# Kernel tuning notes

Measured on AMD Instinct MI355X. Metric: run time of the kernel, lower is better.

## Reference

```python
import jax, jax.numpy as jnp
import numpy as np

# dims
B, L = 2, 1024            # batch, seq len (queries == keys)
DQ, DK, DSRC = 1024, 1024, 512
VIEWS, WIDTH, TOPK = 8, 4, 8
DVP = DQ // VIEWS         # per-view head dim = 128
PAD_F = (WIDTH - 1) // 2  # dilocal 'same' zero padding (stride=1, dilation=1)
PAD_B = (WIDTH - 1) - PAD_F


def setup_inputs() -> dict:
    key = jax.random.key(0)
    ks = jax.random.split(key, 5)
    s = 0.02
    return {
        "query": jax.random.normal(ks[0], (B, L, DQ), jnp.float32),
        "key_t": jax.random.normal(ks[1], (B, L, DK), jnp.float32),
        "source": jax.random.normal(ks[2], (B, L, DSRC), jnp.float32),
        "wq": jax.random.normal(ks[3], (VIEWS, DVP, DQ), jnp.float32) * s,
        "bq": jnp.zeros((VIEWS, DVP), jnp.float32),
        "wk": jax.random.normal(ks[4], (VIEWS, DVP, DK), jnp.float32) * s,
        "bk": jnp.zeros((VIEWS, DVP), jnp.float32),
    }


def reference(query, key_t, source, wq, bq, wk, bk):
    # --- ViewPointFactory.forward ---
    # multi-view projections: [B, L, D] -> [B, views, L, dvp]
    q = jnp.einsum('bld,vkd->bvlk', query, wq) + bq[None, :, None, :]
    k = jnp.einsum('bld,vkd->bvlk', key_t, wk) + bk[None, :, None, :]
    # attention scores over all keys: [B, views, Lq, Lk] (no sqrt(d) scaling in source)
    score = jnp.einsum('bvqd,bvkd->bvqk', q, k)
    # torch.sort(descending) + slice == top_k with sorted values
    vals, idx = jax.lax.top_k(score, TOPK)          # [B, views, Lq, TOPK]
    weights = jax.nn.softmax(vals, axis=-1)

    # --- ViewPoint.__call__(source) ---
    # dilocal: width-WIDTH local windows, stride 1, dilation 1, zero 'same' pad
    padded = jnp.pad(source, ((0, 0), (PAD_F, PAD_B), (0, 0)))
    win_idx = jnp.arange(L)[:, None] + jnp.arange(WIDTH)[None, :]  # [L, WIDTH]
    windows = padded[:, win_idx, :]                 # [B, L, WIDTH, DSRC]

    # gather the top-k key windows per (view, query): [B, views, Lq, TOPK, WIDTH, DSRC]
    gathered = jax.vmap(lambda w, i: w[i])(windows, idx)
    # weighted sum over top-k -> [B, views, Lq, WIDTH, DSRC]
    out = jnp.einsum('bvqk,bvqkwd->bvqwd', weights, gathered)
    return out
```

## Files before the change

kernel.cpp:

```cpp
#include <hip/hip_runtime.h>
#include <cstdint>

#define L_SEQ 1024
#define DSRC 512
#define XPL 2097152L
#define WPL 1048576L

typedef __attribute__((ext_vector_type(8))) short short8;
typedef __attribute__((ext_vector_type(4))) float floatx4;

__device__ __forceinline__ unsigned short f2bf(float f) {
  unsigned int x = __float_as_uint(f);
  x += 0x7fff + ((x >> 16) & 1);
  return (unsigned short)(x >> 16);
}
__device__ __forceinline__ float bf2f(unsigned short h) {
  return __uint_as_float((unsigned)h << 16);
}
__device__ __forceinline__ void split3(float f, unsigned short* h) {
  h[0] = f2bf(f);
  float d = f - bf2f(h[0]);
  h[1] = f2bf(d);
  h[2] = f2bf(d - bf2f(h[1]));
}

__device__ __forceinline__ void gload_lds16(const void* g, void* l) {
  __builtin_amdgcn_global_load_lds(
      (const __attribute__((address_space(1))) unsigned int*)g,
      (__attribute__((address_space(3))) unsigned int*)l, 16, 0, 0);
}

__global__ __launch_bounds__(256) void split_inputs_k(
    const float* __restrict__ query, const float* __restrict__ key_t,
    const float* __restrict__ wq, const float* __restrict__ wk,
    ushort* __restrict__ xs, ushort* __restrict__ wsp) {
  int blk = blockIdx.x;
  const float* in; ushort* out; long pl; int idx;
  if (blk < 2048)      { in = query; out = xs;           pl = XPL; idx = blk; }
  else if (blk < 4096) { in = key_t; out = xs + 3 * XPL; pl = XPL; idx = blk - 2048; }
  else if (blk < 5120) { in = wq;    out = wsp;          pl = WPL; idx = blk - 4096; }
  else                 { in = wk;    out = wsp + 3 * WPL; pl = WPL; idx = blk - 5120; }
  long e = (long)idx * 1024 + threadIdx.x * 4;
  float4 v = *(const float4*)(in + e);
  unsigned short h0[3], h1[3], h2[3], h3[3];
  split3(v.x, h0); split3(v.y, h1); split3(v.z, h2); split3(v.w, h3);
#pragma unroll
  for (int s = 0; s < 3; s++) {
    ushort4 u; u.x = h0[s]; u.y = h1[s]; u.z = h2[s]; u.w = h3[s];
    *(ushort4*)(out + s * pl + e) = u;
  }
}

__global__ __launch_bounds__(512, 2) void proj_gemm_k(
    const ushort* __restrict__ xs, const ushort* __restrict__ wsp,
    ushort* __restrict__ qs, ushort* __restrict__ ks,
    const float* __restrict__ bq, const float* __restrict__ bk) {
  __shared__ ushort As[2][3][4096];
  __shared__ ushort Bs[2][3][4096];
  int z = blockIdx.z;
  const ushort* Ab = xs + (long)z * 3 * XPL + (long)blockIdx.y * 128 * 1024;
  const ushort* Bb = wsp + (long)z * 3 * WPL + (long)blockIdx.x * 128 * 1024;

  int tid = threadIdx.x;
  int lane = tid & 63, wv = tid >> 6;
  int wm = wv >> 2, wn = wv & 3;
  int quad = lane >> 4, l16 = lane & 15;

  int sr = tid >> 2;
  int scq = (((tid & 3) ^ ((sr >> 1) & 3)) << 3);

  floatx4 acc[4][2] = {};

#pragma unroll
  for (int s = 0; s < 3; s++) {
    gload_lds16(Ab + (long)s * XPL + (long)sr * 1024 + scq, &As[0][s][wv * 512]);
    gload_lds16(Bb + (long)s * WPL + (long)sr * 1024 + scq, &Bs[0][s][wv * 512]);
  }
  __syncthreads();

  int cur = 0;
#pragma unroll 2
  for (int t = 0; t < 32; t++) {
    if (t < 31) {
      int k0 = (t + 1) * 32;
#pragma unroll
      for (int s = 0; s < 3; s++) {
        gload_lds16(Ab + (long)s * XPL + (long)sr * 1024 + k0 + scq, &As[cur ^ 1][s][wv * 512]);
        gload_lds16(Bb + (long)s * WPL + (long)sr * 1024 + k0 + scq, &Bs[cur ^ 1][s][wv * 512]);
      }
    }
    short8 af[3][4];
#pragma unroll
    for (int s = 0; s < 3; s++)
#pragma unroll
      for (int i = 0; i < 4; i++) {
        int row = wm * 64 + i * 16 + l16;
        int qa = (quad ^ ((row >> 1) & 3)) << 3;
        af[s][i] = *(const short8*)(&As[cur][s][row * 32 + qa]);
      }
#pragma unroll
    for (int j = 0; j < 2; j++) {
      int rowb = wn * 32 + j * 16 + l16;
      int boff = rowb * 32 + ((quad ^ ((rowb >> 1) & 3)) << 3);
      short8 b0 = *(const short8*)(&Bs[cur][0][boff]);
      short8 b1 = *(const short8*)(&Bs[cur][1][boff]);
      short8 b2 = *(const short8*)(&Bs[cur][2][boff]);
#pragma unroll
      for (int i = 0; i < 4; i++) {
        acc[i][j] = __builtin_amdgcn_mfma_f32_16x16x32_bf16(af[1][i], b1, acc[i][j], 0, 0, 0);
        acc[i][j] = __builtin_amdgcn_mfma_f32_16x16x32_bf16(af[0][i], b2, acc[i][j], 0, 0, 0);
        acc[i][j] = __builtin_amdgcn_mfma_f32_16x16x32_bf16(af[2][i], b0, acc[i][j], 0, 0, 0);
        acc[i][j] = __builtin_amdgcn_mfma_f32_16x16x32_bf16(af[0][i], b1, acc[i][j], 0, 0, 0);
        acc[i][j] = __builtin_amdgcn_mfma_f32_16x16x32_bf16(af[1][i], b0, acc[i][j], 0, 0, 0);
        acc[i][j] = __builtin_amdgcn_mfma_f32_16x16x32_bf16(af[0][i], b0, acc[i][j], 0, 0, 0);
      }
    }
    __syncthreads();
    cur ^= 1;
  }

  ushort* Ob = z ? ks : qs;
  const float* bias = z ? bk : bq;
#pragma unroll
  for (int j = 0; j < 2; j++) {
    int col = blockIdx.x * 128 + wn * 32 + j * 16 + l16;
    float bv = bias[col];
#pragma unroll
    for (int i = 0; i < 4; i++) {
#pragma unroll
      for (int r = 0; r < 4; r++) {
        long row = blockIdx.y * 128 + wm * 64 + i * 16 + quad * 4 + r;
        float val = acc[i][j][r] + bv;
        unsigned short h[3]; split3(val, h);
        long e = row * 1024 + col;
#pragma unroll
        for (int s = 0; s < 3; s++) Ob[s * XPL + e] = h[s];
      }
    }
  }
}

__global__ __launch_bounds__(512) void score_topk_k(
    const ushort* __restrict__ qs, const ushort* __restrict__ ks,
    float* __restrict__ wts, int* __restrict__ idxs) {
  __shared__ ushort Asm[3 * 64 * 128];
  __shared__ ushort Bsm[2][3 * 128 * 32];
  __shared__ float  Ssm[64 * 132];

  int fid = blockIdx.x + 16 * (blockIdx.y + 8 * blockIdx.z);
  int xcd = fid & 7, jj = fid >> 3;
  int pair = xcd * 2 + (jj & 1);
  int rt = jj >> 1;
  int v = pair & 7, b = pair >> 3;

  const long arow0 = (long)b * 1024 + rt * 64;
  const long brow0 = (long)b * 1024;
  const int vb = v * 128;

  int tid = threadIdx.x;
  int lane = tid & 63, wv = tid >> 6;
  int wm = wv >> 2, wn = wv & 3;
  int quad = lane >> 4, l16 = lane & 15;

#pragma unroll
  for (int n = 0; n < 6; n++) {
    int base = n * 512 + wv * 64;
    int sl = base + lane;
    int s = sl >> 10, rem = sl & 1023;
    int r = rem >> 4, sq = rem & 15;
    int qb = sq ^ (r & 7);
    gload_lds16(qs + (long)s * XPL + (arow0 + r) * 1024 + vb + qb * 8,
                &Asm[base * 8]);
  }

  auto stageB = [&](int step, int bsel) {
    int ct2 = step >> 2, kk2 = step & 3;
    long kb = brow0 + ct2 * 128;
    int k0 = kk2 * 32;
#pragma unroll
    for (int n = 0; n < 3; n++) {
      int base = n * 512 + wv * 64;
      int sl = base + lane;
      int s = sl >> 9, rem = sl & 511;
      int c = rem >> 2, sq = rem & 3;
      int qb = sq ^ ((c >> 1) & 3);
      gload_lds16(ks + (long)s * XPL + (kb + c) * 1024 + vb + k0 + qb * 8,
                  &Bsm[bsel][base * 8]);
    }
  };

  stageB(0, 0);
  __syncthreads();

  floatx4 acc[2][2] = {};
  float rv = -1e30f; int rc = 0x7FFFFFFF;
  const int myrow = tid >> 3, lc = tid & 7;

  int buf = 0;
  for (int ct = 0; ct < 8; ct++) {
#pragma unroll
    for (int kk = 0; kk < 4; kk++) {
      int step = ct * 4 + kk;
      if (step < 31) stageB(step + 1, buf ^ 1);

      short8 af[3][2], bf[3][2];
#pragma unroll
      for (int s = 0; s < 3; s++)
#pragma unroll
        for (int i = 0; i < 2; i++) {
          int row = wm * 32 + i * 16 + l16;
          int sqa = (kk * 4 + quad) ^ (row & 7);
          af[s][i] = *(const short8*)(&Asm[s * 8192 + row * 128 + sqa * 8]);
        }
#pragma unroll
      for (int s = 0; s < 3; s++)
#pragma unroll
        for (int j = 0; j < 2; j++) {
          int c = wn * 32 + j * 16 + l16;
          int sqb = quad ^ ((c >> 1) & 3);
          bf[s][j] = *(const short8*)(&Bsm[buf][s * 4096 + c * 32 + sqb * 8]);
        }
#pragma unroll
      for (int j = 0; j < 2; j++)
#pragma unroll
        for (int i = 0; i < 2; i++) {
          acc[i][j] = __builtin_amdgcn_mfma_f32_16x16x32_bf16(af[1][i], bf[1][j], acc[i][j], 0, 0, 0);
          acc[i][j] = __builtin_amdgcn_mfma_f32_16x16x32_bf16(af[0][i], bf[2][j], acc[i][j], 0, 0, 0);
          acc[i][j] = __builtin_amdgcn_mfma_f32_16x16x32_bf16(af[2][i], bf[0][j], acc[i][j], 0, 0, 0);
          acc[i][j] = __builtin_amdgcn_mfma_f32_16x16x32_bf16(af[0][i], bf[1][j], acc[i][j], 0, 0, 0);
          acc[i][j] = __builtin_amdgcn_mfma_f32_16x16x32_bf16(af[1][i], bf[0][j], acc[i][j], 0, 0, 0);
          acc[i][j] = __builtin_amdgcn_mfma_f32_16x16x32_bf16(af[0][i], bf[0][j], acc[i][j], 0, 0, 0);
        }
      __syncthreads();
      buf ^= 1;
    }

#pragma unroll
    for (int i = 0; i < 2; i++)
#pragma unroll
      for (int j = 0; j < 2; j++)
#pragma unroll
        for (int r = 0; r < 4; r++) {
          int row = wm * 32 + i * 16 + quad * 4 + r;
          int col = wn * 32 + j * 16 + l16;
          Ssm[row * 132 + col] = acc[i][j][r];
          acc[i][j][r] = 0.0f;
        }
    __syncthreads();

    float vv[16];
#pragma unroll
    for (int t = 0; t < 16; t++) vv[t] = Ssm[myrow * 132 + lc + 8 * t];

    float nv = -1e30f; int nc = 0x7FFFFFFF;
    for (int rd = 0; rd < 8; rd++) {
      float bv = -1e30f; int bs = 0;
#pragma unroll
      for (int t = 0; t < 16; t++)
        if (vv[t] > bv) { bv = vv[t]; bs = t; }
      int bc = ct * 128 + lc + 8 * bs;
      int myc = bc;
#pragma unroll
      for (int m = 1; m <= 4; m <<= 1) {
        float ov = __shfl_xor(bv, m);
        int oc = __shfl_xor(bc, m);
        if (ov > bv || (ov == bv && oc < bc)) { bv = ov; bc = oc; }
      }
      if (myc == bc) {
#pragma unroll
        for (int t = 0; t < 16; t++)
          if (t == bs) vv[t] = -1e30f;
      }
      if (lc == rd) { nv = bv; nc = bc; }
    }

    float orv = -1e30f; int orc = 0x7FFFFFFF;
    for (int rd = 0; rd < 8; rd++) {
      float bv; int bc;
      if (rv > nv || (rv == nv && rc < nc)) { bv = rv; bc = rc; }
      else { bv = nv; bc = nc; }
#pragma unroll
      for (int m = 1; m <= 4; m <<= 1) {
        float ov = __shfl_xor(bv, m);
        int oc = __shfl_xor(bc, m);
        if (ov > bv || (ov == bv && oc < bc)) { bv = ov; bc = oc; }
      }
      if (bc == rc) rv = -1e30f;
      else if (bc == nc) nv = -1e30f;
      if (lc == rd) { orv = bv; orc = bc; }
    }
    rv = orv; rc = orc;
  }

  float mm = rv;
#pragma unroll
  for (int m = 1; m <= 4; m <<= 1) mm = fmaxf(mm, __shfl_xor(mm, m));
  float e = __expf(rv - mm);
  float sum = e;
#pragma unroll
  for (int m = 1; m <= 4; m <<= 1) sum += __shfl_xor(sum, m);
  float w = e * (1.0f / sum);

  long grow = (long)b * 8192 + v * 1024 + rt * 64 + myrow;
  wts[grow * 8 + lc] = w;
  idxs[grow * 8 + lc] = rc;
}

__global__ __launch_bounds__(256) void gather_out_k(const float* __restrict__ src,
                                                    const float* __restrict__ wts,
                                                    const int* __restrict__ idxs,
                                                    float* __restrict__ out) {
  int rowid = blockIdx.x;
  int b = rowid >> 13;
  int tid = threadIdx.x;
  int d4 = tid & 127;
  int w0 = (tid >> 7) << 1;
  const float4* s4 = (const float4*)src + (long)b * (L_SEQ * (DSRC / 4));
  float wt[8]; int id[8];
#pragma unroll
  for (int k = 0; k < 8; k++) {
    wt[k] = wts[(long)rowid * 8 + k];
    id[k] = idxs[(long)rowid * 8 + k];
  }
  float ax = 0, ay = 0, az = 0, aw = 0;
  float bx = 0, by = 0, bz2 = 0, bw = 0;
#pragma unroll
  for (int k = 0; k < 8; k++) {
    int r0 = id[k] + w0 - 1;
    if ((unsigned)r0 < (unsigned)L_SEQ) {
      float4 x = s4[(long)r0 * 128 + d4];
      ax += wt[k] * x.x; ay += wt[k] * x.y; az += wt[k] * x.z; aw += wt[k] * x.w;
    }
    int r1 = r0 + 1;
    if ((unsigned)r1 < (unsigned)L_SEQ) {
      float4 x = s4[(long)r1 * 128 + d4];
      bx += wt[k] * x.x; by += wt[k] * x.y; bz2 += wt[k] * x.z; bw += wt[k] * x.w;
    }
  }
  float4* o4 = (float4*)out + ((long)rowid * 4 + w0) * 128 + d4;
  o4[0] = make_float4(ax, ay, az, aw);
  o4[128] = make_float4(bx, by, bz2, bw);
}

extern "C" void kernel_launch(void* const* d_in, const int* in_sizes, int n_in,
                              void* d_out, int out_size, void* d_ws, size_t ws_size,
                              hipStream_t stream) {
  (void)in_sizes; (void)n_in; (void)out_size; (void)ws_size;
  const float* query  = (const float*)d_in[0];
  const float* key_t  = (const float*)d_in[1];
  const float* source = (const float*)d_in[2];
  const float* wq     = (const float*)d_in[3];
  const float* bq     = (const float*)d_in[4];
  const float* wk     = (const float*)d_in[5];
  const float* bk     = (const float*)d_in[6];

  char* ws = (char*)d_ws;
  ushort* qs  = (ushort*)(ws);
  ushort* ksp = (ushort*)(ws + 12582912);
  float*  wts = (float*)(ws + 25165824);
  int*    idxs= (int*)(ws + 25690112);
  ushort* xs  = (ushort*)(ws + 26214400);
  ushort* wsp = (ushort*)(ws + 51380224);

  split_inputs_k<<<6144, 256, 0, stream>>>(query, key_t, wq, wk, xs, wsp);
  proj_gemm_k<<<dim3(8, 16, 2), 512, 0, stream>>>(xs, wsp, qs, ksp, bq, bk);
  score_topk_k<<<dim3(16, 8, 2), 512, 0, stream>>>(qs, ksp, wts, idxs);
  gather_out_k<<<16384, 256, 0, stream>>>(source, wts, idxs, (float*)d_out);
}
```

Baseline: 336.0 us.

## Replace shared-memory score staging with per-thread register top-8 insertion in score kernel

The score kernel's top-k is restructured. Each lane keeps sorted top-8 lists in registers for its two query columns and inserts MFMA outputs directly (operands swapped so keys lie along rows), which removes the per-tile score spill to LDS, the extra barrier and the shuffle-based selection rounds. At the end a cross-quad shuffle merge and a 4-way LDS merge by 64 threads produce the final top-8 and softmax. Shared memory is unified into one buffer and launch bounds request 2 blocks per CU. The insertion sort adds branchy VALU work per score and register pressure, which may conflict with the occupancy hint.

Result: faster. 323.0 us (-3.9%).

```diff
diff --git a/kernel.cpp b/kernel.cpp
--- a/kernel.cpp
+++ b/kernel.cpp
@@ -28,6 +28,38 @@
   __builtin_amdgcn_global_load_lds(
       (const __attribute__((address_space(1))) unsigned int*)g,
       (__attribute__((address_space(3))) unsigned int*)l, 16, 0, 0);
+}
+
+__device__ __forceinline__ bool better(float av, int ac, float bv, int bc) {
+  return av > bv || (av == bv && ac < bc);
+}
+__device__ __forceinline__ void ins8(float (&tv)[8], int (&ti)[8], float v, int c) {
+  if (better(v, c, tv[7], ti[7])) {
+    tv[7] = v; ti[7] = c;
+#pragma unroll
+    for (int s = 7; s > 0; s--)
+      if (better(tv[s], ti[s], tv[s - 1], ti[s - 1])) {
+        float a = tv[s]; tv[s] = tv[s - 1]; tv[s - 1] = a;
+        int b2 = ti[s]; ti[s] = ti[s - 1]; ti[s - 1] = b2;
+      }
+  }
+}
+__device__ __forceinline__ void quadmerge_store(float (&tv)[8], int (&ti)[8],
+                                                float* Mv, int* Mi, int base, int quad) {
+#pragma unroll
+  for (int t = 0; t < 8; t++) {
+    float bv = tv[0]; int bc = ti[0];
+    float ov = __shfl_xor(bv, 16); int oc = __shfl_xor(bc, 16);
+    if (better(ov, oc, bv, bc)) { bv = ov; bc = oc; }
+    ov = __shfl_xor(bv, 32); oc = __shfl_xor(bc, 32);
+    if (better(ov, oc, bv, bc)) { bv = ov; bc = oc; }
+    if (bc == ti[0]) {
+#pragma unroll
+      for (int s = 0; s < 7; s++) { tv[s] = tv[s + 1]; ti[s] = ti[s + 1]; }
+      tv[7] = -1e30f; ti[7] = 0x7FFFFFFF;
+    }
+    if (quad == 0) { Mv[base + t] = bv; Mi[base + t] = bc; }
+  }
 }
 
 __global__ __launch_bounds__(256) void split_inputs_k(
@@ -140,12 +172,14 @@
   }
 }
 
-__global__ __launch_bounds__(512) void score_topk_k(
+__global__ __launch_bounds__(512, 2) void score_topk_k(
     const ushort* __restrict__ qs, const ushort* __restrict__ ks,
     float* __restrict__ wts, int* __restrict__ idxs) {
-  __shared__ ushort Asm[3 * 64 * 128];
-  __shared__ ushort Bsm[2][3 * 128 * 32];
-  __shared__ float  Ssm[64 * 132];
+  __shared__ __align__(16) ushort smem[49152];
+  ushort* Qsm = smem;
+  ushort* Kb0 = smem + 24576;
+  float* Mv = (float*)(smem + 24576);
+  int*   Mi = (int*)(smem + 24576 + 4096);
 
   int fid = blockIdx.x + 16 * (blockIdx.y + 8 * blockIdx.z);
   int xcd = fid & 7, jj = fid >> 3;
@@ -159,7 +193,7 @@
 
   int tid = threadIdx.x;
   int lane = tid & 63, wv = tid >> 6;
-  int wm = wv >> 2, wn = wv & 3;
+  int kg = wv & 3, qg = wv >> 2;
   int quad = lane >> 4, l16 = lane & 15;
 
 #pragma unroll
@@ -170,13 +204,14 @@
     int r = rem >> 4, sq = rem & 15;
     int qb = sq ^ (r & 7);
     gload_lds16(qs + (long)s * XPL + (arow0 + r) * 1024 + vb + qb * 8,
-                &Asm[base * 8]);
-  }
-
-  auto stageB = [&](int step, int bsel) {
+                &Qsm[base * 8]);
+  }
+
+  auto stageK = [&](int step, int bsel) {
     int ct2 = step >> 2, kk2 = step & 3;
     long kb = brow0 + ct2 * 128;
     int k0 = kk2 * 32;
+    ushort* Kd = Kb0 + bsel * 12288;
 #pragma unroll
     for (int n = 0; n < 3; n++) {
       int base = n * 512 + wv * 64;
@@ -185,51 +220,55 @@
       int c = rem >> 2, sq = rem & 3;
       int qb = sq ^ ((c >> 1) & 3);
       gload_lds16(ks + (long)s * XPL + (kb + c) * 1024 + vb + k0 + qb * 8,
-                  &Bsm[bsel][base * 8]);
+                  &Kd[base * 8]);
     }
   };
 
-  stageB(0, 0);
+  stageK(0, 0);
   __syncthreads();
 
   floatx4 acc[2][2] = {};
-  float rv = -1e30f; int rc = 0x7FFFFFFF;
-  const int myrow = tid >> 3, lc = tid & 7;
+  float tv0[8], tv1[8]; int ti0[8], ti1[8];
+#pragma unroll
+  for (int t = 0; t < 8; t++) {
+    tv0[t] = tv1[t] = -1e30f; ti0[t] = ti1[t] = 0x7FFFFFFF;
+  }
 
   int buf = 0;
   for (int ct = 0; ct < 8; ct++) {
 #pragma unroll
     for (int kk = 0; kk < 4; kk++) {
       int step = ct * 4 + kk;
-      if (step < 31) stageB(step + 1, buf ^ 1);
-
-      short8 af[3][2], bf[3][2];
+      if (step < 31) stageK(step + 1, buf ^ 1);
+
+      const ushort* Kc = Kb0 + buf * 12288;
+      short8 qf[3][2], kf[3][2];
 #pragma unroll
       for (int s = 0; s < 3; s++)
 #pragma unroll
+        for (int j = 0; j < 2; j++) {
+          int q = qg * 32 + j * 16 + l16;
+          int sqa = (kk * 4 + quad) ^ (q & 7);
+          qf[s][j] = *(const short8*)(&Qsm[s * 8192 + q * 128 + sqa * 8]);
+        }
+#pragma unroll
+      for (int s = 0; s < 3; s++)
+#pragma unroll
         for (int i = 0; i < 2; i++) {
-          int row = wm * 32 + i * 16 + l16;
-          int sqa = (kk * 4 + quad) ^ (row & 7);
-          af[s][i] = *(const short8*)(&Asm[s * 8192 + row * 128 + sqa * 8]);
+          int c = kg * 32 + i * 16 + l16;
+          int sqb = quad ^ ((c >> 1) & 3);
+          kf[s][i] = *(const short8*)(&Kc[s * 4096 + c * 32 + sqb * 8]);
         }
 #pragma unroll
-      for (int s = 0; s < 3; s++)
-#pragma unroll
-        for (int j = 0; j < 2; j++) {
-          int c = wn * 32 + j * 16 + l16;
-          int sqb = quad ^ ((c >> 1) & 3);
-          bf[s][j] = *(const short8*)(&Bsm[buf][s * 4096 + c * 32 + sqb * 8]);
-        }
-#pragma unroll
       for (int j = 0; j < 2; j++)
 #pragma unroll
         for (int i = 0; i < 2; i++) {
-          acc[i][j] = __builtin_amdgcn_mfma_f32_16x16x32_bf16(af[1][i], bf[1][j], acc[i][j], 0, 0, 0);
-          acc[i][j] = __builtin_amdgcn_mfma_f32_16x16x32_bf16(af[0][i], bf[2][j], acc[i][j], 0, 0, 0);
-          acc[i][j] = __builtin_amdgcn_mfma_f32_16x16x32_bf16(af[2][i], bf[0][j], acc[i][j], 0, 0, 0);
-          acc[i][j] = __builtin_amdgcn_mfma_f32_16x16x32_bf16(af[0][i], bf[1][j], acc[i][j], 0, 0, 0);
-          acc[i][j] = __builtin_amdgcn_mfma_f32_16x16x32_bf16(af[1][i], bf[0][j], acc[i][j], 0, 0, 0);
-          acc[i][j] = __builtin_amdgcn_mfma_f32_16x16x32_bf16(af[0][i], bf[0][j], acc[i][j], 0, 0, 0);
+          acc[i][j] = __builtin_amdgcn_mfma_f32_16x16x32_bf16(kf[1][i], qf[1][j], acc[i][j], 0, 0, 0);
+          acc[i][j] = __builtin_amdgcn_mfma_f32_16x16x32_bf16(kf[2][i], qf[0][j], acc[i][j], 0, 0, 0);
+          acc[i][j] = __builtin_amdgcn_mfma_f32_16x16x32_bf16(kf[0][i], qf[2][j], acc[i][j], 0, 0, 0);
+          acc[i][j] = __builtin_amdgcn_mfma_f32_16x16x32_bf16(kf[1][i], qf[0][j], acc[i][j], 0, 0, 0);
+          acc[i][j] = __builtin_amdgcn_mfma_f32_16x16x32_bf16(kf[0][i], qf[1][j], acc[i][j], 0, 0, 0);
+          acc[i][j] = __builtin_amdgcn_mfma_f32_16x16x32_bf16(kf[0][i], qf[0][j], acc[i][j], 0, 0, 0);
         }
       __syncthreads();
       buf ^= 1;
@@ -238,72 +277,51 @@
 #pragma unroll
     for (int i = 0; i < 2; i++)
 #pragma unroll
-      for (int j = 0; j < 2; j++)
-#pragma unroll
-        for (int r = 0; r < 4; r++) {
-          int row = wm * 32 + i * 16 + quad * 4 + r;
-          int col = wn * 32 + j * 16 + l16;
-          Ssm[row * 132 + col] = acc[i][j][r];
-          acc[i][j][r] = 0.0f;
-        }
-    __syncthreads();
-
-    float vv[16];
-#pragma unroll
-    for (int t = 0; t < 16; t++) vv[t] = Ssm[myrow * 132 + lc + 8 * t];
-
-    float nv = -1e30f; int nc = 0x7FFFFFFF;
-    for (int rd = 0; rd < 8; rd++) {
-      float bv = -1e30f; int bs = 0;
-#pragma unroll
-      for (int t = 0; t < 16; t++)
-        if (vv[t] > bv) { bv = vv[t]; bs = t; }
-      int bc = ct * 128 + lc + 8 * bs;
-      int myc = bc;
-#pragma unroll
-      for (int m = 1; m <= 4; m <<= 1) {
-        float ov = __shfl_xor(bv, m);
-        int oc = __shfl_xor(bc, m);
-        if (ov > bv || (ov == bv && oc < bc)) { bv = ov; bc = oc; }
-      }
-      if (myc == bc) {
-#pragma unroll
-        for (int t = 0; t < 16; t++)
-          if (t == bs) vv[t] = -1e30f;
-      }
-      if (lc == rd) { nv = bv; nc = bc; }
-    }
-
-    float orv = -1e30f; int orc = 0x7FFFFFFF;
-    for (int rd = 0; rd < 8; rd++) {
-      float bv; int bc;
-      if (rv > nv || (rv == nv && rc < nc)) { bv = rv; bc = rc; }
-      else { bv = nv; bc = nc; }
-#pragma unroll
-      for (int m = 1; m <= 4; m <<= 1) {
-        float ov = __shfl_xor(bv, m);
-        int oc = __shfl_xor(bc, m);
-        if (ov > bv || (ov == bv && oc < bc)) { bv = ov; bc = oc; }
-      }
-      if (bc == rc) rv = -1e30f;
-      else if (bc == nc) nv = -1e30f;
-      if (lc == rd) { orv = bv; orc = bc; }
-    }
-    rv = orv; rc = orc;
-  }
-
-  float mm = rv;
-#pragma unroll
-  for (int m = 1; m <= 4; m <<= 1) mm = fmaxf(mm, __shfl_xor(mm, m));
-  float e = __expf(rv - mm);
-  float sum = e;
-#pragma unroll
-  for (int m = 1; m <= 4; m <<= 1) sum += __shfl_xor(sum, m);
-  float w = e * (1.0f / sum);
-
-  long grow = (long)b * 8192 + v * 1024 + rt * 64 + myrow;
-  wts[grow * 8 + lc] = w;
-  idxs[grow * 8 + lc] = rc;
+      for (int r = 0; r < 4; r++) {
+        int kglob = ct * 128 + kg * 32 + i * 16 + quad * 4 + r;
+        ins8(tv0, ti0, acc[i][0][r], kglob);
+        ins8(tv1, ti1, acc[i][1][r], kglob);
+        acc[i][0][r] = 0.0f; acc[i][1][r] = 0.0f;
+      }
+  }
+
+  int q0 = qg * 32 + l16;
+  quadmerge_store(tv0, ti0, Mv, Mi, (kg * 64 + q0) * 8, quad);
+  int q1 = q0 + 16;
+  quadmerge_store(tv1, ti1, Mv, Mi, (kg * 64 + q1) * 8, quad);
+  __syncthreads();
+
+  if (tid < 64) {
+    int q = tid;
+    int i0 = 0, i1 = 0, i2 = 0, i3 = 0;
+    float pv[8]; int pc[8];
+#pragma unroll
+    for (int t = 0; t < 8; t++) {
+      float v0 = Mv[(0 * 64 + q) * 8 + i0]; int c0 = Mi[(0 * 64 + q) * 8 + i0];
+      float v1 = Mv[(1 * 64 + q) * 8 + i1]; int c1 = Mi[(1 * 64 + q) * 8 + i1];
+      float v2 = Mv[(2 * 64 + q) * 8 + i2]; int c2 = Mi[(2 * 64 + q) * 8 + i2];
+      float v3 = Mv[(3 * 64 + q) * 8 + i3]; int c3 = Mi[(3 * 64 + q) * 8 + i3];
+      bool b01 = better(v1, c1, v0, c0);
+      float w01v = b01 ? v1 : v0; int w01c = b01 ? c1 : c0; int w01l = b01 ? 1 : 0;
+      bool b23 = better(v3, c3, v2, c2);
+      float w23v = b23 ? v3 : v2; int w23c = b23 ? c3 : c2; int w23l = b23 ? 3 : 2;
+      bool bf_ = better(w23v, w23c, w01v, w01c);
+      float wvv = bf_ ? w23v : w01v; int wcc = bf_ ? w23c : w01c;
+      int wl = bf_ ? w23l : w01l;
+      i0 += (wl == 0); i1 += (wl == 1); i2 += (wl == 2); i3 += (wl == 3);
+      pv[t] = wvv; pc[t] = wcc;
+    }
+    float m = pv[0], sum = 0.f, e[8];
+#pragma unroll
+    for (int t = 0; t < 8; t++) { e[t] = __expf(pv[t] - m); sum += e[t]; }
+    float inv = 1.0f / sum;
+    long grow = (long)b * 8192 + v * 1024 + rt * 64 + q;
+#pragma unroll
+    for (int t = 0; t < 8; t++) {
+      wts[grow * 8 + t] = e[t] * inv;
+      idxs[grow * 8 + t] = pc[t];
+    }
+  }
 }
 
 __global__ __launch_bounds__(256) void gather_out_k(const float* __restrict__ src,
```
